# Kernel tuning notes

Measured on AMD Instinct MI355X. Metric: run time of the kernel, lower is better.

## Reference

```python
import jax, jax.numpy as jnp
import numpy as np


def _lovasz_softmax_flat(probas, labels):
    # probas: [P, C] softmax probabilities; labels: [P] int class ids
    P, C = probas.shape
    classes = jnp.arange(C)
    # fg[c, p] = 1 if pixel p has ground-truth class c
    fg = (labels[None, :] == classes[:, None]).astype(probas.dtype)      # [C, P]
    errors = jnp.abs(fg - probas.T)                                       # [C, P]
    # sort errors descending per class, permute fg the same way
    order = jnp.argsort(-errors, axis=1)                                  # [C, P]
    errors_sorted = jnp.take_along_axis(errors, order, axis=1)
    fg_sorted = jnp.take_along_axis(fg, order, axis=1)
    # Lovasz gradient of the Jaccard loss w.r.t. sorted errors
    gts = jnp.sum(fg_sorted, axis=1, keepdims=True)                       # [C, 1]
    intersection = gts - jnp.cumsum(fg_sorted, axis=1)
    union = gts + jnp.cumsum(1.0 - fg_sorted, axis=1)
    jaccard = 1.0 - intersection / union                                  # [C, P]
    jaccard = jnp.concatenate([jaccard[:, :1], jaccard[:, 1:] - jaccard[:, :-1]], axis=1)
    # grad is treated as constant w.r.t. probas (matches torch Variable(grad) detach)
    jaccard = jax.lax.stop_gradient(jaccard)
    losses = jnp.sum(errors_sorted * jaccard, axis=1)                     # [C]
    # classes='present': average only over classes present in the labels
    present = (gts[:, 0] > 0).astype(probas.dtype)
    return jnp.sum(losses * present) / jnp.maximum(jnp.sum(present), 1.0)


def reference(input, target):
    B, C, H, W = input.shape
    probas = jax.nn.softmax(input, axis=1)                                # [B, C, H, W]
    probas_flat = probas.transpose(0, 2, 3, 1).reshape(-1, C)             # [P, C]
    labels_flat = target.reshape(-1)                                      # [P]
    return _lovasz_softmax_flat(probas_flat, labels_flat)


def setup_inputs() -> dict:
    key = jax.random.key(0)
    k1, k2 = jax.random.split(key)
    B, C, H, W = 8, 19, 512, 512
    inp = jax.random.normal(k1, (B, C, H, W), dtype=jnp.float32)
    tgt = jax.random.randint(k2, (B, H, W), 0, C, dtype=jnp.int64)
    return {"input": inp, "target": tgt}
```

## Files before the change

### kernel.cpp

```cpp
#include <hip/hip_runtime.h>
#include <stdint.h>


#define C_CLASSES 19
#define NBINS 768
#define HISTWORDS (C_CLASSES * NBINS)
#define HW_SHIFT 18
#define HW_MASK ((1 << HW_SHIFT) - 1)
#define NGROUPS 8

__global__ __launch_bounds__(1024) void k1_hist(
    const float* __restrict__ x, const int* __restrict__ labels,
    unsigned int* __restrict__ copies, int P, int pixPerBlk)
{
    __shared__ unsigned int hist[HISTWORDS];
    int tid = threadIdx.x;
    for (int i = tid; i < HISTWORDS; i += 1024) hist[i] = 0u;
    __syncthreads();

    int base = blockIdx.x * pixPerBlk;
    for (int it = 0; it < pixPerBlk; it += 1024) {
        int p = base + it + tid;
        if (p < P) {
            int lab = labels[p];
            int img = p >> HW_SHIFT;
            int rem = p & HW_MASK;
            const float* xp = x + (((size_t)img * C_CLASSES) << HW_SHIFT) + rem;
            float r[C_CLASSES];
            float m = -1e30f;
#pragma unroll
            for (int c = 0; c < C_CLASSES; ++c) {
                r[c] = xp[(size_t)c << HW_SHIFT];
                m = fmaxf(m, r[c]);
            }
            float s = 0.f;
#pragma unroll
            for (int c = 0; c < C_CLASSES; ++c) { r[c] = __expf(r[c] - m); s += r[c]; }
            float inv = 1.f / s;
#pragma unroll
            for (int c = 0; c < C_CLASSES; ++c) {
                float pr = r[c] * inv;
                bool fg = (c == lab);
                float err = fg ? (1.f - pr) : pr;
                int idx = __float2int_rn(err * (float)(NBINS - 1));
                idx = idx < 0 ? 0 : (idx > NBINS - 1 ? NBINS - 1 : idx);
                atomicAdd(&hist[c * NBINS + idx], fg ? 0x10001u : 1u);
            }
        }
    }
    __syncthreads();
    unsigned int* dst = copies + (size_t)blockIdx.x * HISTWORDS;
    for (int i = tid; i < HISTWORDS; i += 1024) dst[i] = hist[i];
}

__global__ __launch_bounds__(256) void k2_reduce(
    const unsigned int* __restrict__ copies,
    int* __restrict__ nPart, int* __restrict__ fPart,
    int ncopies, int cpg)
{
    int pos = blockIdx.x * 256 + threadIdx.x;
    int g = blockIdx.y;
    int c0 = g * cpg;
    int c1 = c0 + cpg; if (c1 > ncopies) c1 = ncopies;
    unsigned int sn = 0, sf = 0;
    for (int k = c0; k < c1; ++k) {
        unsigned int w = copies[(size_t)k * HISTWORDS + pos];
        sn += w & 0xFFFFu;
        sf += w >> 16;
    }
    nPart[(size_t)g * HISTWORDS + pos] = (int)sn;
    fPart[(size_t)g * HISTWORDS + pos] = (int)sf;
}

__global__ __launch_bounds__(64) void k3_scan(
    const int* __restrict__ nPart, const int* __restrict__ fPart,
    float* __restrict__ res)
{
    int c = blockIdx.x;
    int lane = threadIdx.x;
    const int PER = NBINS / 64;
    int nl[PER], fl[PER];
    int totN = 0, totF = 0;
#pragma unroll
    for (int i = 0; i < PER; ++i) {
        int j = lane * PER + i;
        int bin = NBINS - 1 - j;
        int pos = c * NBINS + bin;
        int n = 0, f = 0;
#pragma unroll
        for (int g = 0; g < NGROUPS; ++g) {
            n += nPart[g * HISTWORDS + pos];
            f += fPart[g * HISTWORDS + pos];
        }
        nl[i] = n; fl[i] = f; totN += n; totF += f;
    }
    int incN = totN, incF = totF;
    for (int off = 1; off < 64; off <<= 1) {
        int tn = __shfl_up(incN, off);
        int tf = __shfl_up(incF, off);
        if (lane >= off) { incN += tn; incF += tf; }
    }
    int G = __shfl(incF, 63);
    double loss = 0.0;
    if (G > 0) {
        int cumN = incN - totN;
        int cumF = incF - totF;
        double dG = (double)G;
        double Jb = 1.0 - (dG - (double)cumF) / (dG + (double)cumN - (double)cumF);
#pragma unroll
        for (int i = 0; i < PER; ++i) {
            int bin = NBINS - 1 - (lane * PER + i);
            cumN += nl[i]; cumF += fl[i];
            double Ja = 1.0 - (dG - (double)cumF) / (dG + (double)cumN - (double)cumF);
            loss += ((double)bin / (double)(NBINS - 1)) * (Ja - Jb);
            Jb = Ja;
        }
    }
    for (int off = 32; off > 0; off >>= 1)
        loss += __shfl_down(loss, off);
    if (lane == 0) { res[c] = (float)loss; res[C_CLASSES + c] = (float)G; }
}

__global__ void k4_final(const float* __restrict__ res, float* __restrict__ out)
{
    if (threadIdx.x == 0 && blockIdx.x == 0) {
        float s = 0.f, cnt = 0.f;
        for (int c = 0; c < C_CLASSES; ++c) {
            if (res[C_CLASSES + c] > 0.f) { s += res[c]; cnt += 1.f; }
        }
        out[0] = s / fmaxf(cnt, 1.f);
    }
}

extern "C" void kernel_launch(void* const* d_in, const int* in_sizes, int n_in,
                              void* d_out, int out_size, void* d_ws, size_t ws_size,
                              hipStream_t stream)
{
    const float* x = (const float*)d_in[0];
    const int* labels = (const int*)d_in[1];
    float* out = (float*)d_out;
    int P = in_sizes[1];

    const size_t histBytes = (size_t)HISTWORDS * 4;
    const size_t partBytes = (size_t)NGROUPS * HISTWORDS * 4;
    const size_t resBytes = 2 * C_CLASSES * 4;
    const size_t reserved = 2 * partBytes + resBytes + 256;

    int maxCopies = (int)((ws_size > reserved ? ws_size - reserved : 0) / histBytes);
    int ncopies = maxCopies < 512 ? maxCopies : 512;
    if (ncopies < 1) ncopies = 1;
    int pixPerBlk = (P + ncopies - 1) / ncopies;
    pixPerBlk = ((pixPerBlk + 1023) / 1024) * 1024;

    unsigned int* copies = (unsigned int*)d_ws;
    int* nPart = (int*)((char*)d_ws + histBytes * (size_t)ncopies);
    int* fPart = (int*)((char*)nPart + partBytes);
    float* res = (float*)((char*)fPart + partBytes);

    int cpg = (ncopies + NGROUPS - 1) / NGROUPS;

    k1_hist<<<dim3(ncopies), dim3(1024), 0, stream>>>(x, labels, copies, P, pixPerBlk);
    k2_reduce<<<dim3(HISTWORDS / 256, NGROUPS), dim3(256), 0, stream>>>(copies, nPart, fPart, ncopies, cpg);
    k3_scan<<<dim3(C_CLASSES), dim3(64), 0, stream>>>(nPart, fPart, res);
    k4_final<<<dim3(1), dim3(64), 0, stream>>>(res, out);
}
```

Before: 254.6 us.

## Merge block histograms via global atomics and fuse scan with final reduction

```diff
diff --git a/kernel.cpp b/kernel.cpp
--- a/kernel.cpp
+++ b/kernel.cpp
@@ -11,7 +11,7 @@
 
 __global__ __launch_bounds__(1024) void k1_hist(
     const float* __restrict__ x, const int* __restrict__ labels,
-    unsigned int* __restrict__ copies, int P, int pixPerBlk)
+    int* __restrict__ nGlob, int* __restrict__ fGlob, int P, int pixPerBlk)
 {
     __shared__ unsigned int hist[HISTWORDS];
     int tid = threadIdx.x;
@@ -44,90 +44,82 @@
                 float err = fg ? (1.f - pr) : pr;
                 int idx = __float2int_rn(err * (float)(NBINS - 1));
                 idx = idx < 0 ? 0 : (idx > NBINS - 1 ? NBINS - 1 : idx);
-                atomicAdd(&hist[c * NBINS + idx], fg ? 0x10001u : 1u);
+                if (idx != 0 || fg)
+                    atomicAdd(&hist[c * NBINS + idx], fg ? 0x10001u : 1u);
             }
         }
     }
     __syncthreads();
-    unsigned int* dst = copies + (size_t)blockIdx.x * HISTWORDS;
-    for (int i = tid; i < HISTWORDS; i += 1024) dst[i] = hist[i];
+    int g = blockIdx.x & (NGROUPS - 1);
+    int* nG = nGlob + (size_t)g * HISTWORDS;
+    int* fG = fGlob + (size_t)g * HISTWORDS;
+    for (int i = tid; i < HISTWORDS; i += 1024) {
+        unsigned int w = hist[i];
+        unsigned int n = w & 0xFFFFu;
+        unsigned int f = w >> 16;
+        if (n) atomicAdd(&nG[i], (int)n);
+        if (f) atomicAdd(&fG[i], (int)f);
+    }
 }
 
-__global__ __launch_bounds__(256) void k2_reduce(
-    const unsigned int* __restrict__ copies,
-    int* __restrict__ nPart, int* __restrict__ fPart,
-    int ncopies, int cpg)
+__global__ __launch_bounds__(1024) void k2_scan(
+    const int* __restrict__ nGlob, const int* __restrict__ fGlob,
+    float* __restrict__ out)
 {
-    int pos = blockIdx.x * 256 + threadIdx.x;
-    int g = blockIdx.y;
-    int c0 = g * cpg;
-    int c1 = c0 + cpg; if (c1 > ncopies) c1 = ncopies;
-    unsigned int sn = 0, sf = 0;
-    for (int k = c0; k < c1; ++k) {
-        unsigned int w = copies[(size_t)k * HISTWORDS + pos];
-        sn += w & 0xFFFFu;
-        sf += w >> 16;
-    }
-    nPart[(size_t)g * HISTWORDS + pos] = (int)sn;
-    fPart[(size_t)g * HISTWORDS + pos] = (int)sf;
-}
+    __shared__ float resL[32];
+    __shared__ float gL[32];
+    int tid = threadIdx.x;
+    int wave = tid >> 6;
+    int lane = tid & 63;
 
-__global__ __launch_bounds__(64) void k3_scan(
-    const int* __restrict__ nPart, const int* __restrict__ fPart,
-    float* __restrict__ res)
-{
-    int c = blockIdx.x;
-    int lane = threadIdx.x;
-    const int PER = NBINS / 64;
-    int nl[PER], fl[PER];
-    int totN = 0, totF = 0;
-#pragma unroll
-    for (int i = 0; i < PER; ++i) {
-        int j = lane * PER + i;
-        int bin = NBINS - 1 - j;
-        int pos = c * NBINS + bin;
-        int n = 0, f = 0;
-#pragma unroll
-        for (int g = 0; g < NGROUPS; ++g) {
-            n += nPart[g * HISTWORDS + pos];
-            f += fPart[g * HISTWORDS + pos];
-        }
-        nl[i] = n; fl[i] = f; totN += n; totF += f;
-    }
-    int incN = totN, incF = totF;
-    for (int off = 1; off < 64; off <<= 1) {
-        int tn = __shfl_up(incN, off);
-        int tf = __shfl_up(incF, off);
-        if (lane >= off) { incN += tn; incF += tf; }
-    }
-    int G = __shfl(incF, 63);
-    double loss = 0.0;
-    if (G > 0) {
-        int cumN = incN - totN;
-        int cumF = incF - totF;
-        double dG = (double)G;
-        double Jb = 1.0 - (dG - (double)cumF) / (dG + (double)cumN - (double)cumF);
+    for (int c = wave; c < C_CLASSES; c += 16) {
+        const int PER = NBINS / 64;
+        int nl[PER], fl[PER];
+        int totN = 0, totF = 0;
 #pragma unroll
         for (int i = 0; i < PER; ++i) {
-            int bin = NBINS - 1 - (lane * PER + i);
-            cumN += nl[i]; cumF += fl[i];
-            double Ja = 1.0 - (dG - (double)cumF) / (dG + (double)cumN - (double)cumF);
-            loss += ((double)bin / (double)(NBINS - 1)) * (Ja - Jb);
-            Jb = Ja;
+            int j = lane * PER + i;
+            int bin = NBINS - 1 - j;
+            int pos = c * NBINS + bin;
+            int n = 0, f = 0;
+#pragma unroll
+            for (int g = 0; g < NGROUPS; ++g) {
+                n += nGlob[g * HISTWORDS + pos];
+                f += fGlob[g * HISTWORDS + pos];
+            }
+            nl[i] = n; fl[i] = f; totN += n; totF += f;
         }
+        int incN = totN, incF = totF;
+        for (int off = 1; off < 64; off <<= 1) {
+            int tn = __shfl_up(incN, off);
+            int tf = __shfl_up(incF, off);
+            if (lane >= off) { incN += tn; incF += tf; }
+        }
+        int G = __shfl(incF, 63);
+        double loss = 0.0;
+        if (G > 0) {
+            int cumN = incN - totN;
+            int cumF = incF - totF;
+            double dG = (double)G;
+            double Jb = 1.0 - (dG - (double)cumF) / (dG + (double)cumN - (double)cumF);
+#pragma unroll
+            for (int i = 0; i < PER; ++i) {
+                int bin = NBINS - 1 - (lane * PER + i);
+                cumN += nl[i]; cumF += fl[i];
+                double Ja = 1.0 - (dG - (double)cumF) / (dG + (double)cumN - (double)cumF);
+                loss += ((double)bin / (double)(NBINS - 1)) * (Ja - Jb);
+                Jb = Ja;
+            }
+        }
+        for (int off = 32; off > 0; off >>= 1)
+            loss += __shfl_down(loss, off);
+        if (lane == 0) { resL[c] = (float)loss; gL[c] = (float)G; }
     }
-    for (int off = 32; off > 0; off >>= 1)
-        loss += __shfl_down(loss, off);
-    if (lane == 0) { res[c] = (float)loss; res[C_CLASSES + c] = (float)G; }
-}
-
-__global__ void k4_final(const float* __restrict__ res, float* __restrict__ out)
-{
-    if (threadIdx.x == 0 && blockIdx.x == 0) {
+    __syncthreads();
+    if (tid == 0) {
         float s = 0.f, cnt = 0.f;
-        for (int c = 0; c < C_CLASSES; ++c) {
-            if (res[C_CLASSES + c] > 0.f) { s += res[c]; cnt += 1.f; }
-        }
+        for (int c = 0; c < C_CLASSES; ++c)
+            if (gL[c] > 0.f) { s += resL[c]; cnt += 1.f; }
         out[0] = s / fmaxf(cnt, 1.f);
     }
 }
@@ -141,26 +133,16 @@
     float* out = (float*)d_out;
     int P = in_sizes[1];
 
-    const size_t histBytes = (size_t)HISTWORDS * 4;
-    const size_t partBytes = (size_t)NGROUPS * HISTWORDS * 4;
-    const size_t resBytes = 2 * C_CLASSES * 4;
-    const size_t reserved = 2 * partBytes + resBytes + 256;
+    const size_t partWords = (size_t)NGROUPS * HISTWORDS;
+    int* nGlob = (int*)d_ws;
+    int* fGlob = nGlob + partWords;
 
-    int maxCopies = (int)((ws_size > reserved ? ws_size - reserved : 0) / histBytes);
-    int ncopies = maxCopies < 512 ? maxCopies : 512;
-    if (ncopies < 1) ncopies = 1;
-    int pixPerBlk = (P + ncopies - 1) / ncopies;
+    hipMemsetAsync(d_ws, 0, 2 * partWords * sizeof(int), stream);
+
+    const int NBLOCKS = 512;
+    int pixPerBlk = (P + NBLOCKS - 1) / NBLOCKS;
     pixPerBlk = ((pixPerBlk + 1023) / 1024) * 1024;
 
-    unsigned int* copies = (unsigned int*)d_ws;
-    int* nPart = (int*)((char*)d_ws + histBytes * (size_t)ncopies);
-    int* fPart = (int*)((char*)nPart + partBytes);
-    float* res = (float*)((char*)fPart + partBytes);
-
-    int cpg = (ncopies + NGROUPS - 1) / NGROUPS;
-
-    k1_hist<<<dim3(ncopies), dim3(1024), 0, stream>>>(x, labels, copies, P, pixPerBlk);
-    k2_reduce<<<dim3(HISTWORDS / 256, NGROUPS), dim3(256), 0, stream>>>(copies, nPart, fPart, ncopies, cpg);
-    k3_scan<<<dim3(C_CLASSES), dim3(64), 0, stream>>>(nPart, fPart, res);
-    k4_final<<<dim3(1), dim3(64), 0, stream>>>(res, out);
+    k1_hist<<<dim3(NBLOCKS), dim3(1024), 0, stream>>>(x, labels, nGlob, fGlob, P, pixPerBlk);
+    k2_scan<<<dim3(1), dim3(1024), 0, stream>>>(nGlob, fGlob, out);
 }
```

After: 260.9 us. +2.5%, slower.
